# Optimization experiments

Measured on AMD Instinct MI355X. Metric: run time of the kernel, lower is better.

Reference implementation:

```python
import jax, jax.numpy as jnp
import numpy as np

B, T, C, H, R = 2, 2048, 2048, 16, 8
D = C // H  # head_dim = 128


def _rope_cache(seq_len, dim, theta=10000.0):
    pos = jnp.arange(seq_len, dtype=jnp.float32)[:, None]            # [T,1]
    idx = jnp.arange(0, dim, 2, dtype=jnp.float32)                   # [D/2]
    freqs = 1.0 / (theta ** (idx / dim))
    ang = pos * freqs                                                # [T, D/2]
    return jnp.cos(ang), jnp.sin(ang)


def setup_inputs() -> dict:
    key = jax.random.key(0)
    ks = jax.random.split(key, 16)
    s = 0.02
    inp = {"x": jax.random.normal(ks[0], (B, T, C), dtype=jnp.float32)}
    i = 1
    for nm in ("q", "k", "v", "p"):
        inp[f"{nm}_w"] = jax.random.normal(ks[i], (C, C), dtype=jnp.float32) * s; i += 1
        inp[f"{nm}_b"] = jnp.zeros((C,), dtype=jnp.float32)
        inp[f"{nm}_A"] = jax.random.normal(ks[i], (C, R), dtype=jnp.float32) * s; i += 1
        inp[f"{nm}_B"] = jax.random.normal(ks[i], (R, C), dtype=jnp.float32) * s; i += 1
    cos, sin = _rope_cache(T, D)
    inp["cos"] = cos
    inp["sin"] = sin
    inp["mask"] = jnp.tril(jnp.ones((T, T), dtype=bool))  # causal SDPA mask
    inp["use_lora"] = 1
    return inp


def _lora_linear(x, w, b, A, Bm, use_lora):
    # base GEMM + bias, plus low-rank adapter x @ A @ B (intended path)
    out = x @ w.T + b
    if use_lora:
        out = out + (x @ A) @ Bm
    return out


def _apply_rope(x, cos, sin):
    # x: [B,H,T,D]; cos/sin: [T, D/2] broadcast over batch & heads
    x1 = x[..., ::2]
    x2 = x[..., 1::2]
    y = jnp.stack((x1 * cos - x2 * sin, x1 * sin + x2 * cos), axis=-1)
    return y.reshape(x.shape)


def reference(x, q_w, q_b, q_A, q_B, k_w, k_b, k_A, k_B,
              v_w, v_b, v_A, v_B, p_w, p_b, p_A, p_B,
              cos, sin, mask, use_lora):
    Bsz, Tl, Cd = x.shape
    q = _lora_linear(x, q_w, q_b, q_A, q_B, use_lora).reshape(Bsz, Tl, H, D).transpose(0, 2, 1, 3)
    k = _lora_linear(x, k_w, k_b, k_A, k_B, use_lora).reshape(Bsz, Tl, H, D).transpose(0, 2, 1, 3)
    v = _lora_linear(x, v_w, v_b, v_A, v_B, use_lora).reshape(Bsz, Tl, H, D).transpose(0, 2, 1, 3)
    q = _apply_rope(q, cos, sin)
    k = _apply_rope(k, cos, sin)
    # scaled dot-product attention with boolean mask (True = attend)
    scale = 1.0 / jnp.sqrt(jnp.asarray(D, dtype=x.dtype))
    scores = jnp.einsum('bhqd,bhkd->bhqk', q, k) * scale          # [B,H,T,T]
    neg = jnp.asarray(jnp.finfo(scores.dtype).min, dtype=scores.dtype)
    scores = jnp.where(mask, scores, neg)
    attn = jax.nn.softmax(scores, axis=-1)
    out = jnp.einsum('bhqk,bhkd->bhqd', attn, v)                  # [B,H,T,D]
    y = out.transpose(0, 2, 1, 3).reshape(Bsz, Tl, Cd)
    return _lora_linear(y, p_w, p_b, p_A, p_B, use_lora)
```

## Files before the change

kernel.cpp:

```cpp
#include <hip/hip_runtime.h>

typedef _Float16 f16;
typedef _Float16 f16x4 __attribute__((ext_vector_type(4)));
typedef _Float16 f16x8 __attribute__((ext_vector_type(8)));
typedef __fp16 hf2 __attribute__((ext_vector_type(2)));
typedef float f32x4 __attribute__((ext_vector_type(4)));

#define DEV static __device__ __forceinline__

DEV void gl_lds16(const void* g, void* l) {
  __builtin_amdgcn_global_load_lds(
      (const __attribute__((address_space(1))) void*)g,
      (__attribute__((address_space(3))) void*)l, 16, 0, 0);
}

DEV uint pkrtz(float a, float b) {
  hf2 h = __builtin_amdgcn_cvt_pkrtz(a, b);
  return __builtin_bit_cast(uint, h);
}

DEV f32x4 MFMA(f16x8 a, f16x8 b, f32x4 c) {
  return __builtin_amdgcn_mfma_f32_16x16x32_f16(a, b, c, 0, 0, 0);
}

#define SC2Q 0.12752551286084103f

__global__ __launch_bounds__(256) void prep_kernel(
    const float* __restrict__ x, f16* __restrict__ xb,
    const float* __restrict__ w0, const float* __restrict__ A0,
    const float* __restrict__ B0, f16* __restrict__ o0,
    const float* __restrict__ w1, const float* __restrict__ A1,
    const float* __restrict__ B1, f16* __restrict__ o1,
    const float* __restrict__ w2, const float* __restrict__ A2,
    const float* __restrict__ B2, f16* __restrict__ o2,
    const float* __restrict__ w3, const float* __restrict__ A3,
    const float* __restrict__ B3, f16* __restrict__ o3,
    const int* __restrict__ use_lora) {
  const float ul = (float)use_lora[0];
  const int gid = blockIdx.x * 256 + threadIdx.x;
  const int stride = gridDim.x * 256;
  const int XF4 = 2097152;
  const int WF4 = 1048576;

  for (int i = gid; i < XF4; i += stride) {
    float4 v = ((const float4*)x)[i];
    f16x4 h = {(f16)v.x, (f16)v.y, (f16)v.z, (f16)v.w};
    ((f16x4*)xb)[i] = h;
  }

  const float* Ws[4] = {w0, w1, w2, w3};
  const float* As[4] = {A0, A1, A2, A3};
  const float* Bs[4] = {B0, B1, B2, B3};
  f16* Os[4] = {o0, o1, o2, o3};
#pragma unroll
  for (int wsel = 0; wsel < 4; ++wsel) {
    const float* W = Ws[wsel];
    const float* A = As[wsel];
    const float* Bm = Bs[wsel];
    f16* O = Os[wsel];
    for (int i = gid; i < WF4; i += stride) {
      const int n = i >> 9;
      const int k = (i & 511) << 2;
      float4 wv = ((const float4*)W)[i];
      float bcol[8];
#pragma unroll
      for (int r = 0; r < 8; ++r) bcol[r] = Bm[r * 2048 + n];
      const float4* Ap = (const float4*)(A + (size_t)k * 8);
      float ov[4];
      const float* wp = &wv.x;
#pragma unroll
      for (int j = 0; j < 4; ++j) {
        float4 a0 = Ap[j * 2], a1 = Ap[j * 2 + 1];
        float s = a0.x * bcol[0] + a0.y * bcol[1] + a0.z * bcol[2] +
                  a0.w * bcol[3] + a1.x * bcol[4] + a1.y * bcol[5] +
                  a1.z * bcol[6] + a1.w * bcol[7];
        ov[j] = wp[j] + ul * s;
      }
      f16x4 h = {(f16)ov[0], (f16)ov[1], (f16)ov[2], (f16)ov[3]};
      ((f16x4*)O)[i] = h;
    }
  }
}

struct GemmArgs {
  const f16* A;
  const f16* W[3];
  const float* bias[3];
  void* out[3];
  int mode[3];
};

__global__ __launch_bounds__(256, 2) void gemm2_kernel(
    GemmArgs args, const float* __restrict__ cosT,
    const float* __restrict__ sinT) {
  extern __shared__ char smem[];
  const int z = blockIdx.y;
  const f16* A = args.A;
  const f16* Bw = args.W[z];
  const float* bias = args.bias[z];
  void* out = args.out[z];
  const int mode = args.mode[z];

  const int tid = threadIdx.x;
  const int wave = tid >> 6, lane = tid & 63;
  const int lr = lane & 15, lg = lane >> 4;
  const int bm = (int)blockIdx.x >> 4, bn = (int)blockIdx.x & 15;
  const int m0 = bm << 7, n0 = bn << 7;
  const int wr = wave >> 1, wc = wave & 1;

  const char* Ab = (const char*)A;
  const char* Bb = (const char*)Bw;

  uint aoff[4], boff[4];
#pragma unroll
  for (int r = 0; r < 4; ++r) {
    uint beta = (uint)(wave * 4 + r) * 1024 + (uint)lane * 16;
    uint row = beta >> 7;
    uint c = (beta & 127u) ^ ((row & 7u) << 4);
    aoff[r] = (uint)(m0 + row) * 4096 + c;
    boff[r] = (uint)(n0 + row) * 4096 + c;
  }

  auto STAGE = [&](int kt, int b) {
    char* dst = smem + b * 32768;
    const size_t kb = (size_t)kt << 7;
#pragma unroll
    for (int r = 0; r < 4; ++r) {
      gl_lds16(Ab + (aoff[r] + kb), dst + (wave * 4 + r) * 1024);
      gl_lds16(Bb + (boff[r] + kb), dst + 16384 + (wave * 4 + r) * 1024);
    }
  };

  f32x4 acc[4][4] = {};

  STAGE(0, 0);
  for (int kt = 0; kt < 32; ++kt) {
    const int b = kt & 1;
    asm volatile("s_waitcnt vmcnt(0) lgkmcnt(0)" ::: "memory");
    __builtin_amdgcn_s_barrier();
    if (kt + 1 < 32) STAGE(kt + 1, b ^ 1);

    const char* buf = smem + b * 32768;
    f16x8 af[2][4], bf[2][4];
#pragma unroll
    for (int ks = 0; ks < 2; ++ks) {
#pragma unroll
      for (int mi = 0; mi < 4; ++mi) {
        int row = wr * 64 + mi * 16 + lr;
        int c = (ks * 64 + lg * 16) ^ ((row & 7) << 4);
        af[ks][mi] = *(const f16x8*)(buf + row * 128 + c);
      }
#pragma unroll
      for (int ni = 0; ni < 4; ++ni) {
        int row = wc * 64 + ni * 16 + lr;
        int c = (ks * 64 + lg * 16) ^ ((row & 7) << 4);
        bf[ks][ni] = *(const f16x8*)(buf + 16384 + row * 128 + c);
      }
    }
    __builtin_amdgcn_s_setprio(1);
#pragma unroll
    for (int ks = 0; ks < 2; ++ks)
#pragma unroll
      for (int mi = 0; mi < 4; ++mi)
#pragma unroll
        for (int ni = 0; ni < 4; ++ni)
          acc[mi][ni] = MFMA(af[ks][mi], bf[ks][ni], acc[mi][ni]);
    __builtin_amdgcn_s_setprio(0);
  }

  asm volatile("s_waitcnt lgkmcnt(0)" ::: "memory");
  __builtin_amdgcn_s_barrier();

  float bv[4];
#pragma unroll
  for (int ni = 0; ni < 4; ++ni) bv[ni] = bias[n0 + wc * 64 + ni * 16 + lr];

#pragma unroll
  for (int mi = 0; mi < 4; ++mi) {
    const int mbase = m0 + wr * 64 + mi * 16 + lg * 4;
#pragma unroll
    for (int ni = 0; ni < 4; ++ni) {
      const int n = n0 + wc * 64 + ni * 16 + lr;
#pragma unroll
      for (int rg = 0; rg < 4; ++rg) {
        float v = acc[mi][ni][rg] + bv[ni];
        const int mm = wr * 64 + mi * 16 + lg * 4 + rg;
        const int nn = wc * 64 + ni * 16 + lr;
        if (mode <= 1) {
          float pv = __shfl_xor(v, 1);
          const int t = (mbase + rg) & 2047;
          const int ci = t * 64 + ((n & 127) >> 1);
          float cs = cosT[ci], sn = sinT[ci];
          float res = ((lane & 1) == 0) ? (v * cs - pv * sn)
                                        : (pv * sn + v * cs);
          if (mode == 0) res *= SC2Q;
          ((f16*)smem)[mm * 128 + nn] = (f16)res;
        } else if (mode == 2) {
          *(f16*)(smem + nn * 256 + ((mm * 2) ^ ((nn & 7) << 4))) = (f16)v;
        } else {
          ((float*)out)[(size_t)(mbase + rg) * 2048 + n] = v;
        }
      }
    }
  }

  if (mode <= 1) {
    __builtin_amdgcn_s_barrier();
    const long b_ = m0 >> 11;
    const int tb = m0 & 2047;
    char* obase = (char*)out + ((b_ * 16 + bn) * 2048 + tb) * 256;
#pragma unroll
    for (int p = 0; p < 8; ++p) {
      int s = p * 4096 + tid * 16;
      int row = s >> 8, c = s & 255;
      *(uint4*)(obase + (long)row * 256 + c) = *(const uint4*)(smem + s);
    }
  } else if (mode == 2) {
    __builtin_amdgcn_s_barrier();
    const long b_ = m0 >> 11;
    const int tb = m0 & 2047;
    char* obase = (char*)out + (((b_ * 16 + bn) * 128) * 2048 + tb) * 2;
#pragma unroll
    for (int p = 0; p < 8; ++p) {
      int s = p * 4096 + tid * 16;
      int row = s >> 8, cb = s & 255;
      int c = cb ^ ((row & 7) << 4);
      uint4 val = *(const uint4*)(smem + row * 256 + c);
      *(uint4*)(obase + (long)row * 4096 + cb) = val;
    }
  }
}

__global__ __launch_bounds__(256, 2) void attn_kernel(
    const f16* __restrict__ qr, const f16* __restrict__ kr,
    const f16* __restrict__ vt, f16* __restrict__ y) {
  extern __shared__ char smem[];
  const int tid = threadIdx.x, wave = tid >> 6, lane = tid & 63;
  const int lr = lane & 15, lg = lane >> 4;
  const int qt = 15 - (int)blockIdx.x;
  const int q0 = qt << 7;
  const int h = blockIdx.y, b = blockIdx.z;
  const long bh = b * 16 + h;
  const int nt = 2 * qt + 2;

  const char* kbase = (const char*)kr + bh * 2048 * 256;
  const char* vbase = (const char*)vt + bh * 128 * 4096;

  uint koff[4], voff[4];
#pragma unroll
  for (int r = 0; r < 4; ++r) {
    uint s = (uint)(wave * 4 + r) * 1024 + (uint)lane * 16;
    uint rowk = s >> 8;
    koff[r] = rowk * 256 + ((s & 255u) ^ ((rowk & 7u) << 4));
    uint rowv = s >> 7;
    voff[r] = rowv * 4096 + ((s & 127u) ^ ((rowv & 7u) << 4));
  }

  f16x8 qf[2][4];
#pragma unroll
  for (int g = 0; g < 2; ++g) {
    const char* qb =
        (const char*)qr + (bh * 2048 + q0 + wave * 32 + g * 16 + lr) * 256;
#pragma unroll
    for (int ks = 0; ks < 4; ++ks)
      qf[g][ks] = *(const f16x8*)(qb + ks * 64 + lg * 16);
  }

  f32x4 o[2][8] = {};
  float mrow[2] = {-3e38f, -3e38f};
  float lsum[2] = {0.f, 0.f};

  auto STAGE = [&](int kv0, int bsel) {
    char* Ks = smem + bsel * 32768;
    char* Vs = Ks + 16384;
#pragma unroll
    for (int r = 0; r < 4; ++r) {
      gl_lds16(kbase + (size_t)kv0 * 256 + koff[r], Ks + (wave * 4 + r) * 1024);
      gl_lds16(vbase + (size_t)kv0 * 2 + voff[r], Vs + (wave * 4 + r) * 1024);
    }
  };

  STAGE(0, 0);
  __syncthreads();

  for (int kt = 0; kt < nt; ++kt) {
    const int kv0 = kt << 6;
    if (kt + 1 < nt) STAGE((kt + 1) << 6, (kt + 1) & 1);
    const char* Ks = smem + (kt & 1) * 32768;
    const char* Vs = Ks + 16384;

    if (kv0 <= q0 + wave * 32 + 31) {
      f32x4 sa[2][4] = {};
      __builtin_amdgcn_s_setprio(1);
#pragma unroll
      for (int ks = 0; ks < 4; ++ks)
#pragma unroll
        for (int n = 0; n < 4; ++n) {
          int row = n * 16 + lr;
          int c = (ks * 64 + lg * 16) ^ ((row & 7) << 4);
          f16x8 kf = *(const f16x8*)(Ks + row * 256 + c);
          sa[0][n] = MFMA(kf, qf[0][ks], sa[0][n]);
          sa[1][n] = MFMA(kf, qf[1][ks], sa[1][n]);
        }
      __builtin_amdgcn_s_setprio(0);

      f16x8 pf[2][2];
#pragma unroll
      for (int g = 0; g < 2; ++g) {
        const int qgbase = q0 + wave * 32 + g * 16;
        float L[16];
        const bool dm = (kv0 + 63 > qgbase);
#pragma unroll
        for (int n = 0; n < 4; ++n)
#pragma unroll
          for (int rg = 0; rg < 4; ++rg) {
            float Lv = sa[g][n][rg];
            if (dm && (kv0 + n * 16 + lg * 4 + rg > qgbase + lr)) Lv = -3e37f;
            L[n * 4 + rg] = Lv;
          }
        float m0a = fmaxf(L[0], L[1]),  m1a = fmaxf(L[2], L[3]);
        float m2a = fmaxf(L[4], L[5]),  m3a = fmaxf(L[6], L[7]);
        float m4a = fmaxf(L[8], L[9]),  m5a = fmaxf(L[10], L[11]);
        float m6a = fmaxf(L[12], L[13]), m7a = fmaxf(L[14], L[15]);
        float m0b = fmaxf(m0a, m1a), m1b = fmaxf(m2a, m3a);
        float m2b = fmaxf(m4a, m5a), m3b = fmaxf(m6a, m7a);
        float pm = fmaxf(fmaxf(m0b, m1b), fmaxf(m2b, m3b));
        if (!__all(pm <= mrow[g] + 8.f)) {
          pm = fmaxf(pm, __shfl_xor(pm, 16));
          pm = fmaxf(pm, __shfl_xor(pm, 32));
          float mn = fmaxf(mrow[g], pm);
          float alpha = exp2f(mrow[g] - mn);
          mrow[g] = mn;
          lsum[g] *= alpha;
#pragma unroll
          for (int dt = 0; dt < 8; ++dt)
#pragma unroll
            for (int rg = 0; rg < 4; ++rg) o[g][dt][rg] *= alpha;
        }
        const float mn = mrow[g];
#pragma unroll
        for (int i = 0; i < 16; ++i) L[i] = exp2f(L[i] - mn);
        float s0 = L[0] + L[1], s1 = L[2] + L[3], s2 = L[4] + L[5],
              s3 = L[6] + L[7], s4 = L[8] + L[9], s5 = L[10] + L[11],
              s6 = L[12] + L[13], s7 = L[14] + L[15];
        float t0 = s0 + s1, t1 = s2 + s3, t2 = s4 + s5, t3 = s6 + s7;
        float ps = (t0 + t1) + (t2 + t3);
        ps += __shfl_xor(ps, 16);
        ps += __shfl_xor(ps, 32);
        lsum[g] += ps;

#pragma unroll
        for (int ks2 = 0; ks2 < 2; ++ks2) {
          uint w0 = pkrtz(L[8 * ks2 + 0], L[8 * ks2 + 1]);
          uint w1 = pkrtz(L[8 * ks2 + 2], L[8 * ks2 + 3]);
          uint w2 = pkrtz(L[8 * ks2 + 4], L[8 * ks2 + 5]);
          uint w3 = pkrtz(L[8 * ks2 + 6], L[8 * ks2 + 7]);
          int src1 = ((lg & 1) << 5) + lr;
          int src2 = src1 + 16;
          uint a0 = __shfl((int)w0, src1), a1 = __shfl((int)w1, src1);
          uint a2 = __shfl((int)w2, src1), a3 = __shfl((int)w3, src1);
          uint b0 = __shfl((int)w0, src2), b1 = __shfl((int)w1, src2);
          uint b2 = __shfl((int)w2, src2), b3 = __shfl((int)w3, src2);
          const bool hi = (lg >> 1) != 0;
          uint4 uu;
          uu.x = hi ? a2 : a0;
          uu.y = hi ? a3 : a1;
          uu.z = hi ? b2 : b0;
          uu.w = hi ? b3 : b1;
          pf[g][ks2] = __builtin_bit_cast(f16x8, uu);
        }
      }

#pragma unroll
      for (int ks2 = 0; ks2 < 2; ++ks2) {
        __builtin_amdgcn_s_setprio(1);
#pragma unroll
        for (int dt = 0; dt < 8; ++dt) {
          int drow = dt * 16 + lr;
          int c = (ks2 * 64 + lg * 16) ^ ((drow & 7) << 4);
          f16x8 vf = *(const f16x8*)(Vs + drow * 128 + c);
          o[0][dt] = MFMA(vf, pf[0][ks2], o[0][dt]);
          o[1][dt] = MFMA(vf, pf[1][ks2], o[1][dt]);
        }
        __builtin_amdgcn_s_setprio(0);
      }
    }
    __syncthreads();
  }

#pragma unroll
  for (int g = 0; g < 2; ++g) {
    const float inv = 1.f / lsum[g];
    const int row = wave * 32 + g * 16 + lr;
#pragma unroll
    for (int dt = 0; dt < 8; ++dt) {
      uint lo = pkrtz(o[g][dt][0] * inv, o[g][dt][1] * inv);
      uint hi2 = pkrtz(o[g][dt][2] * inv, o[g][dt][3] * inv);
      int c = (dt * 32 + lg * 8) ^ ((row & 7) << 4);
      uint2 w;
      w.x = lo;
      w.y = hi2;
      *(uint2*)(smem + row * 256 + c) = w;
    }
  }
  __syncthreads();
#pragma unroll
  for (int p = 0; p < 8; ++p) {
    int s = p * 4096 + tid * 16;
    int row = s >> 8, cb = s & 255;
    int c = cb ^ ((row & 7) << 4);
    char* dst =
        (char*)y + ((long)(b * 2048 + q0 + row) * 2048 + h * 128) * 2 + cb;
    *(uint4*)dst = *(const uint4*)(smem + row * 256 + c);
  }
}

extern "C" void kernel_launch(void* const* d_in, const int* in_sizes, int n_in,
                              void* d_out, int out_size, void* d_ws,
                              size_t ws_size, hipStream_t stream) {
  (void)in_sizes; (void)n_in; (void)out_size; (void)ws_size;
  const float* x   = (const float*)d_in[0];
  const float* q_w = (const float*)d_in[1];
  const float* q_b = (const float*)d_in[2];
  const float* q_A = (const float*)d_in[3];
  const float* q_B = (const float*)d_in[4];
  const float* k_w = (const float*)d_in[5];
  const float* k_b = (const float*)d_in[6];
  const float* k_A = (const float*)d_in[7];
  const float* k_B = (const float*)d_in[8];
  const float* v_w = (const float*)d_in[9];
  const float* v_b = (const float*)d_in[10];
  const float* v_A = (const float*)d_in[11];
  const float* v_B = (const float*)d_in[12];
  const float* p_w = (const float*)d_in[13];
  const float* p_b = (const float*)d_in[14];
  const float* p_A = (const float*)d_in[15];
  const float* p_B = (const float*)d_in[16];
  const float* cosT = (const float*)d_in[17];
  const float* sinT = (const float*)d_in[18];
  const int* use_lora = (const int*)d_in[20];

  char* ws = (char*)d_ws;
  f16* xb  = (f16*)(ws);
  f16* wqb = (f16*)(ws + 16777216);
  f16* wkb = (f16*)(ws + 25165824);
  f16* wvb = (f16*)(ws + 33554432);
  f16* wpb = (f16*)(ws + 41943040);
  f16* qr  = (f16*)(ws + 50855936);
  f16* kr  = (f16*)(ws + 67633152);
  f16* vt  = (f16*)(ws + 84410368);
  f16* y   = xb;

  prep_kernel<<<dim3(2048), dim3(256), 0, stream>>>(
      x, xb, q_w, q_A, q_B, wqb, k_w, k_A, k_B, wkb, v_w, v_A, v_B, wvb, p_w,
      p_A, p_B, wpb, use_lora);

  GemmArgs qkv;
  qkv.A = xb;
  qkv.W[0] = wqb;  qkv.W[1] = wkb;  qkv.W[2] = wvb;
  qkv.bias[0] = q_b; qkv.bias[1] = k_b; qkv.bias[2] = v_b;
  qkv.out[0] = qr; qkv.out[1] = kr; qkv.out[2] = vt;
  qkv.mode[0] = 0; qkv.mode[1] = 1; qkv.mode[2] = 2;
  gemm2_kernel<<<dim3(512, 3), dim3(256), 65536, stream>>>(qkv, cosT, sinT);

  attn_kernel<<<dim3(16, 16, 2), dim3(256), 65536, stream>>>(qr, kr, vt, y);

  GemmArgs pp;
  pp.A = y;
  pp.W[0] = wpb;  pp.W[1] = wpb;  pp.W[2] = wpb;
  pp.bias[0] = p_b; pp.bias[1] = p_b; pp.bias[2] = p_b;
  pp.out[0] = d_out; pp.out[1] = d_out; pp.out[2] = d_out;
  pp.mode[0] = 3; pp.mode[1] = 3; pp.mode[2] = 3;
  gemm2_kernel<<<dim3(512, 1), dim3(256), 65536, stream>>>(pp, nullptr,
                                                           nullptr);
}
```

Measured before the change: 345.1 us.

## Load GEMM A operand directly into registers, staging only B through LDS

The GEMM kernel no longer stages the A tile through shared memory. Each wave loads its A fragments straight from global memory into registers, double-buffered across k-steps by a two-step unrolled loop, while only the B tile goes through LDS. This halves LDS use per block (64KB to 32KB), which may allow more resident blocks, and removes the LDS reads for A. In exchange it adds VGPR pressure and uncoalesced per-lane 16-byte global loads, and each A fragment is loaded by both waves that share a row.

```diff
diff --git a/kernel.cpp b/kernel.cpp
--- a/kernel.cpp
+++ b/kernel.cpp
@@ -111,62 +111,72 @@
   const char* Ab = (const char*)A;
   const char* Bb = (const char*)Bw;
 
-  uint aoff[4], boff[4];
+  size_t abase[4];
+#pragma unroll
+  for (int mi = 0; mi < 4; ++mi)
+    abase[mi] =
+        (size_t)(m0 + wr * 64 + mi * 16 + lr) * 4096 + (size_t)lg * 16;
+
+  uint boff[4];
 #pragma unroll
   for (int r = 0; r < 4; ++r) {
     uint beta = (uint)(wave * 4 + r) * 1024 + (uint)lane * 16;
     uint row = beta >> 7;
     uint c = (beta & 127u) ^ ((row & 7u) << 4);
-    aoff[r] = (uint)(m0 + row) * 4096 + c;
     boff[r] = (uint)(n0 + row) * 4096 + c;
   }
 
-  auto STAGE = [&](int kt, int b) {
-    char* dst = smem + b * 32768;
+  auto STAGEB = [&](int kt, int b) {
+    char* dst = smem + b * 16384;
     const size_t kb = (size_t)kt << 7;
 #pragma unroll
-    for (int r = 0; r < 4; ++r) {
-      gl_lds16(Ab + (aoff[r] + kb), dst + (wave * 4 + r) * 1024);
-      gl_lds16(Bb + (boff[r] + kb), dst + 16384 + (wave * 4 + r) * 1024);
-    }
+    for (int r = 0; r < 4; ++r)
+      gl_lds16(Bb + (boff[r] + kb), dst + (wave * 4 + r) * 1024);
   };
 
   f32x4 acc[4][4] = {};
-
-  STAGE(0, 0);
-  for (int kt = 0; kt < 32; ++kt) {
-    const int b = kt & 1;
-    asm volatile("s_waitcnt vmcnt(0) lgkmcnt(0)" ::: "memory");
-    __builtin_amdgcn_s_barrier();
-    if (kt + 1 < 32) STAGE(kt + 1, b ^ 1);
-
-    const char* buf = smem + b * 32768;
-    f16x8 af[2][4], bf[2][4];
-#pragma unroll
-    for (int ks = 0; ks < 2; ++ks) {
-#pragma unroll
-      for (int mi = 0; mi < 4; ++mi) {
-        int row = wr * 64 + mi * 16 + lr;
-        int c = (ks * 64 + lg * 16) ^ ((row & 7) << 4);
-        af[ks][mi] = *(const f16x8*)(buf + row * 128 + c);
-      }
-#pragma unroll
-      for (int ni = 0; ni < 4; ++ni) {
-        int row = wc * 64 + ni * 16 + lr;
-        int c = (ks * 64 + lg * 16) ^ ((row & 7) << 4);
-        bf[ks][ni] = *(const f16x8*)(buf + 16384 + row * 128 + c);
-      }
-    }
-    __builtin_amdgcn_s_setprio(1);
-#pragma unroll
-    for (int ks = 0; ks < 2; ++ks)
-#pragma unroll
-      for (int mi = 0; mi < 4; ++mi)
-#pragma unroll
-        for (int ni = 0; ni < 4; ++ni)
-          acc[mi][ni] = MFMA(af[ks][mi], bf[ks][ni], acc[mi][ni]);
-    __builtin_amdgcn_s_setprio(0);
-  }
+  f16x8 afA[2][4], afB[2][4];
+
+#define LOADA(kt, dst)                                                       \
+  {                                                                          \
+    const size_t kbb = (size_t)(kt) << 7;                                    \
+    _Pragma("unroll") for (int ks = 0; ks < 2; ++ks)                         \
+        _Pragma("unroll") for (int mi = 0; mi < 4; ++mi) dst[ks][mi] =       \
+            *(const f16x8*)(Ab + abase[mi] + kbb + ks * 64);                 \
+  }
+
+#define KSTEP(kt, cur, nxt)                                                  \
+  {                                                                          \
+    asm volatile("s_waitcnt vmcnt(0) lgkmcnt(0)" ::: "memory");              \
+    __builtin_amdgcn_s_barrier();                                            \
+    if ((kt) + 1 < 32) {                                                     \
+      LOADA((kt) + 1, nxt);                                                  \
+      STAGEB((kt) + 1, ((kt) + 1) & 1);                                      \
+    }                                                                        \
+    const char* buf = smem + ((kt)&1) * 16384;                               \
+    f16x8 bf[2][4];                                                          \
+    _Pragma("unroll") for (int ks = 0; ks < 2; ++ks)                         \
+        _Pragma("unroll") for (int ni = 0; ni < 4; ++ni) {                   \
+      int row = wc * 64 + ni * 16 + lr;                                      \
+      int c = (ks * 64 + lg * 16) ^ ((row & 7) << 4);                        \
+      bf[ks][ni] = *(const f16x8*)(buf + row * 128 + c);                     \
+    }                                                                        \
+    __builtin_amdgcn_s_setprio(1);                                           \
+    _Pragma("unroll") for (int ks = 0; ks < 2; ++ks)                         \
+        _Pragma("unroll") for (int mi = 0; mi < 4; ++mi)                     \
+            _Pragma("unroll") for (int ni = 0; ni < 4; ++ni) acc[mi][ni] =   \
+                MFMA(cur[ks][mi], bf[ks][ni], acc[mi][ni]);                  \
+    __builtin_amdgcn_s_setprio(0);                                           \
+  }
+
+  LOADA(0, afA);
+  STAGEB(0, 0);
+  for (int kt2 = 0; kt2 < 32; kt2 += 2) {
+    KSTEP(kt2, afA, afB);
+    KSTEP(kt2 + 1, afB, afA);
+  }
+#undef KSTEP
+#undef LOADA
 
   asm volatile("s_waitcnt lgkmcnt(0)" ::: "memory");
   __builtin_amdgcn_s_barrier();
@@ -461,7 +471,7 @@
   qkv.bias[0] = q_b; qkv.bias[1] = k_b; qkv.bias[2] = v_b;
   qkv.out[0] = qr; qkv.out[1] = kr; qkv.out[2] = vt;
   qkv.mode[0] = 0; qkv.mode[1] = 1; qkv.mode[2] = 2;
-  gemm2_kernel<<<dim3(512, 3), dim3(256), 65536, stream>>>(qkv, cosT, sinT);
+  gemm2_kernel<<<dim3(512, 3), dim3(256), 32768, stream>>>(qkv, cosT, sinT);
 
   attn_kernel<<<dim3(16, 16, 2), dim3(256), 65536, stream>>>(qr, kr, vt, y);
 
@@ -471,6 +481,6 @@
   pp.bias[0] = p_b; pp.bias[1] = p_b; pp.bias[2] = p_b;
   pp.out[0] = d_out; pp.out[1] = d_out; pp.out[2] = d_out;
   pp.mode[0] = 3; pp.mode[1] = 3; pp.mode[2] = 3;
-  gemm2_kernel<<<dim3(512, 1), dim3(256), 65536, stream>>>(pp, nullptr,
+  gemm2_kernel<<<dim3(512, 1), dim3(256), 32768, stream>>>(pp, nullptr,
                                                            nullptr);
 }
```

New measurement: 512.1 us. 1.48x slower.
